# Optimization experiments

Measured on AMD Instinct MI355X. Metric: run time of the kernel, lower is better.

The kernel has to match this reference:

```python
import jax, jax.numpy as jnp
import numpy as np

N = 40000        # total points
B = 4            # batch size
Q = 256          # cfg.n_query_points
N_INSTS = B * Q  # 1024
N_MASK = 30000   # foreground points
L = 6            # cfg.dec_nlayers
LOSS_W3 = 1.0    # cfg.loss_weight[3]


def setup_inputs() -> dict:
    key = jax.random.key(0)
    k1, k2, k3, k4, k5 = jax.random.split(key, 5)
    offsets = (jnp.arange(B + 1, dtype=jnp.int32) * (N // B))
    fg_idxs = jnp.sort(jax.random.randint(k1, (N_MASK,), 0, N))
    batch_idxs = jnp.searchsorted(offsets, fg_idxs.astype(jnp.int32), side='right') - 1
    b_n = jnp.arange(N_INSTS) // Q
    fps_sampling_inds = offsets[b_n].astype(jnp.int64) + jax.random.randint(k2, (N_INSTS,), 0, N // B)
    instance_labels = jax.random.randint(k3, (N,), -1, 40)   # -1 = no instance
    semantic_labels = jax.random.randint(k4, (N,), 0, 20)    # >=4 = thing classes
    mask_logits = jax.random.normal(k5, (L, N_INSTS, N_MASK), dtype=jnp.float32)
    return {
        'mask_logits': mask_logits,
        'semantic_labels': semantic_labels,
        'instance_labels': instance_labels,
        'fg_idxs': fg_idxs,
        'batch_idxs': batch_idxs,
        'offsets': offsets,
        'fps_sampling_inds': fps_sampling_inds,
        'num_insts': N_INSTS,
    }


def reference(mask_logits, semantic_labels, instance_labels, fg_idxs,
              batch_idxs, offsets, fps_sampling_inds, num_insts):
    n_pts = instance_labels.shape[0]
    b_n = jnp.arange(num_insts) // Q                      # batch id of each query
    s_ins = instance_labels[fps_sampling_inds]            # [n_insts]
    s_seg = semantic_labels[fps_sampling_inds]            # [n_insts]
    inst_m = instance_labels[fg_idxs]                     # [n_mask]
    sem_m = semantic_labels[fg_idxs]                      # [n_mask]

    same_batch = batch_idxs[None, :] == b_n[:, None]      # [n_insts, n_mask]
    gt = inst_m[None, :] == s_ins[:, None]                # [n_insts, n_mask]

    # cover_percent: fg-point matches within query batch / all-point matches within batch slice
    num = (same_batch & gt).sum(axis=1)
    pt_batch = jnp.searchsorted(offsets, jnp.arange(n_pts, dtype=jnp.int32), side='right') - 1
    den = ((pt_batch[None, :] == b_n[:, None]) & (instance_labels[None, :] == s_ins[:, None])).sum(axis=1)
    cover = num.astype(jnp.float32) / den.astype(jnp.float32)

    positive = (s_ins >= 0) & (s_seg >= 4) & (cover >= 0.3)
    p = positive.astype(jnp.float32)                      # [n_insts]

    gt_f = gt.astype(jnp.float32)
    # weights: 1 inside own batch, zeroed where semantic label differs; rows only for positives
    w = p[:, None] * (same_batch & (sem_m[None, :] == s_seg[:, None])).astype(jnp.float32)
    w_row = w.sum(axis=1)
    counted = p * (w_row > 0).astype(jnp.float32)         # positives with >=1 valid point

    loss = jnp.float32(0.0)
    for l in range(L - 4, L):
        logit = mask_logits[l]                            # [n_insts, n_mask]
        pred = jax.nn.sigmoid(logit)
        # masked dice (weights are binary -> equals gather-then-dice of original)
        inter = (w * pred * gt_f).sum(axis=1)
        union = (w * pred * pred).sum(axis=1) + (w * gt_f).sum(axis=1) + 1e-5
        dice = 1.0 - 2.0 * inter / union
        dice_loss = (counted * dice).sum() / (counted.sum() + 1e-6)
        # weighted BCE on sigmoid (stable log-sigmoid form)
        bce = -(gt_f * jax.nn.log_sigmoid(logit) + (1.0 - gt_f) * jax.nn.log_sigmoid(-logit))
        score_loss = (bce * w).sum() / (w.sum() + 1e-6)
        loss = loss + LOSS_W3 * score_loss + dice_loss
    return loss
```

## Files before the change

### kernel.cpp

```cpp
#include <hip/hip_runtime.h>
#include <cstddef>
#include <cstdint>

#define SEMB 64
#define INSB 64
#define GRIDN 256
#define BLKN 1024
#define NWAVE 16
#define SUB 2
#define NLOSS 4
#define QPB 4
#define CHK 3840
#define MAGIC 0x5A5A5A5Au

struct Args {
    const float* logits;
    const int *sem, *inst, *fg, *bidx, *offs, *fps;
    int N, NM, NI, B, Qv, L0;
    unsigned int* flags;
    float* bceP;
    float* diceP;
    float* wcP;
    float* out;
};

__global__ __launch_bounds__(BLKN) void k_fused(Args a) {
    const int tid = threadIdx.x;
    const int bid = blockIdx.x;
    const int wid = tid >> 6, lane = tid & 63;

    __shared__ int   hA [INSB * SUB];
    __shared__ int   hFI[INSB * SUB];
    __shared__ int   hFS[SEMB * SUB];
    __shared__ int   sTot[SEMB];
    __shared__ int   lists[QPB][CHK];
    __shared__ int   lcnt[QPB];
    __shared__ int   qPos[QPB], qSi[QPB], qSs[QPB];
    __shared__ int   sFlo, sFhi;
    __shared__ float sRed[NWAVE][13];
    __shared__ float tb[NWAVE][NLOSS], td[NWAVE][NLOSS];
    __shared__ float sWC[2];

    const int b0   = (bid * QPB) / a.Qv;
    const int o_lo = a.offs[b0], o_hi = a.offs[b0 + 1];

    if (tid < INSB * SUB) { hA[tid] = 0; hFI[tid] = 0; }
    else if (tid < INSB * SUB + SEMB * SUB) hFS[tid - INSB * SUB] = 0;
    __syncthreads();

    if (tid < 896) {
        for (int k = o_lo + tid; k < o_hi; k += 896)
            atomicAdd(&hA[(a.inst[k] + 1) * SUB + (tid & (SUB - 1))], 1);
    } else if (tid == 896 || tid == 960) {
        int target = (tid == 896) ? o_lo : o_hi;
        int l_ = 0, h_ = a.NM;
        while (l_ < h_) { int m = (l_ + h_) >> 1; if (a.fg[m] < target) l_ = m + 1; else h_ = m; }
        if (tid == 896) sFlo = l_; else sFhi = l_;
    }
    __syncthreads();
    const int flo = sFlo, fhi = sFhi;

    for (int j = flo + tid; j < fhi; j += BLKN) {
        int f = a.fg[j];
        atomicAdd(&hFI[(a.inst[f] + 1) * SUB + (tid & (SUB - 1))], 1);
        atomicAdd(&hFS[a.sem[f]       * SUB + (tid & (SUB - 1))], 1);
    }
    __syncthreads();

    if (tid < SEMB) {
        int s = 0;
        for (int u = 0; u < SUB; ++u) s += hFS[tid * SUB + u];
        sTot[tid] = s;
    }
    if (tid >= 128 && tid < 128 + QPB) {
        int q = tid - 128;
        int i = bid * QPB + q;
        int pos = 0, si = -1, ss = 0;
        if (i < a.NI) {
            int fi = a.fps[i];
            si = a.inst[fi]; ss = a.sem[fi];
            if (si >= 0 && ss >= 4) {
                int num = 0, den = 0;
                for (int u = 0; u < SUB; ++u) {
                    num += hFI[(si + 1) * SUB + u];
                    den += hA [(si + 1) * SUB + u];
                }
                if ((float)num / (float)den >= 0.3f) pos = 1;
            }
        }
        qPos[q] = pos; qSi[q] = si; qSs[q] = ss;
    }
    __syncthreads();

    const int q = wid >> 2, sub = wid & 3;
    const int iq = bid * QPB + q;
    const size_t stride = (size_t)a.NI * (size_t)a.NM;
    const float* __restrict__ r0 =
        a.logits + ((size_t)a.L0 * a.NI + iq) * (size_t)a.NM;

    float acc[12];
    #pragma unroll
    for (int z = 0; z < 12; ++z) acc[z] = 0.f;
    float nm = 0.f;

    for (int c = flo; c < fhi; c += CHK) {
        int ce = (c + CHK < fhi) ? c + CHK : fhi;
        if (tid < QPB) lcnt[tid] = 0;
        __syncthreads();
        for (int j = c + tid; j < ce; j += BLKN) {
            int f  = a.fg[j];
            int sm = a.sem[f];
            int im = a.inst[f];
            int e  = j | ((im + 1) << 16);
            #pragma unroll
            for (int qq = 0; qq < QPB; ++qq) {
                if (qPos[qq] && sm == qSs[qq]) {
                    int p = atomicAdd(&lcnt[qq], 1);
                    lists[qq][p] = e;
                }
            }
        }
        __syncthreads();
        if (qPos[q]) {
            int cnt = lcnt[q];
            for (int k = (sub << 6) + lane; k < cnt; k += 256) {
                int e = lists[q][k];
                const float* __restrict__ rp = r0 + (e & 0xFFFF);
                bool g = (e >> 16) == qSi[q] + 1;
                if (g) nm += 1.f;
                #pragma unroll
                for (int l = 0; l < NLOSS; ++l) {
                    float x   = rp[(size_t)l * stride];
                    float em  = expf(-fabsf(x));
                    float inv = 1.f / (1.f + em);
                    float sg  = (x >= 0.f) ? inv : em * inv;
                    float bc  = log1pf(em) + fmaxf(x, 0.f);
                    acc[l * 3 + 0] += sg * sg;
                    if (g) { acc[l * 3 + 1] += sg; bc -= x; }
                    acc[l * 3 + 2] += bc;
                }
            }
        }
        __syncthreads();
    }

    #pragma unroll
    for (int off = 32; off > 0; off >>= 1) {
        #pragma unroll
        for (int z = 0; z < 12; ++z) acc[z] += __shfl_down(acc[z], off, 64);
        nm += __shfl_down(nm, off, 64);
    }
    if (lane == 0) {
        #pragma unroll
        for (int z = 0; z < 12; ++z) sRed[wid][z] = acc[z];
        sRed[wid][12] = nm;
    }
    __syncthreads();
    if (tid == 0) {
        float bO[NLOSS] = {0.f, 0.f, 0.f, 0.f};
        float dO[NLOSS] = {0.f, 0.f, 0.f, 0.f};
        float wr = 0.f, ct = 0.f;
        for (int qq = 0; qq < QPB; ++qq) {
            if (!qPos[qq]) continue;
            int w = sTot[qSs[qq]];
            wr += (float)w;
            ct += (w > 0) ? 1.f : 0.f;
            float s[13];
            for (int z = 0; z < 13; ++z)
                s[z] = sRed[qq * 4 + 0][z] + sRed[qq * 4 + 1][z]
                     + sRed[qq * 4 + 2][z] + sRed[qq * 4 + 3][z];
            int counted = w > 0;
            for (int l = 0; l < NLOSS; ++l) {
                bO[l] += s[l * 3 + 2];
                if (counted) {
                    float un = s[l * 3 + 0] + s[12] + 1e-5f;
                    dO[l] += 1.f - 2.f * s[l * 3 + 1] / un;
                }
            }
        }
        #pragma unroll
        for (int l = 0; l < NLOSS; ++l) {
            a.bceP[bid * NLOSS + l]  = bO[l];
            a.diceP[bid * NLOSS + l] = dO[l];
        }
        a.wcP[bid * 2 + 0] = wr;
        a.wcP[bid * 2 + 1] = ct;
        __threadfence();
        __hip_atomic_store(&a.flags[bid], MAGIC,
                           __ATOMIC_RELAXED, __HIP_MEMORY_SCOPE_AGENT);
    }

    if (bid != 0) return;

    if (wid == 0) {
        bool done = false;
        do {
            unsigned v0 = __hip_atomic_load(&a.flags[lane],       __ATOMIC_RELAXED, __HIP_MEMORY_SCOPE_AGENT);
            unsigned v1 = __hip_atomic_load(&a.flags[lane + 64],  __ATOMIC_RELAXED, __HIP_MEMORY_SCOPE_AGENT);
            unsigned v2 = __hip_atomic_load(&a.flags[lane + 128], __ATOMIC_RELAXED, __HIP_MEMORY_SCOPE_AGENT);
            unsigned v3 = __hip_atomic_load(&a.flags[lane + 192], __ATOMIC_RELAXED, __HIP_MEMORY_SCOPE_AGENT);
            done = __all((v0 == MAGIC) && (v1 == MAGIC) && (v2 == MAGIC) && (v3 == MAGIC));
            if (!done) __builtin_amdgcn_s_sleep(8);
        } while (!done);
    }
    __syncthreads();
    __threadfence();

    if (tid < GRIDN) a.flags[tid] = 0;

    float pb = a.bceP[tid], pd = a.diceP[tid];
    #pragma unroll
    for (int off = 32; off >= 4; off >>= 1) {
        pb += __shfl_down(pb, off, 64);
        pd += __shfl_down(pd, off, 64);
    }
    if (lane < NLOSS) { tb[wid][lane] = pb; td[wid][lane] = pd; }
    if (wid == 0) {
        float wv = 0.f, cv = 0.f;
        for (int b = lane; b < GRIDN; b += 64) {
            wv += a.wcP[b * 2 + 0];
            cv += a.wcP[b * 2 + 1];
        }
        #pragma unroll
        for (int off = 32; off > 0; off >>= 1) {
            wv += __shfl_down(wv, off, 64);
            cv += __shfl_down(cv, off, 64);
        }
        if (lane == 0) { sWC[0] = wv; sWC[1] = cv; }
    }
    __syncthreads();
    if (tid == 0) {
        float wsum = sWC[0] + 1e-6f;
        float csum = sWC[1] + 1e-6f;
        float loss = 0.f;
        for (int l = 0; l < NLOSS; ++l) {
            float sb = 0.f, sd = 0.f;
            for (int w = 0; w < NWAVE; ++w) { sb += tb[w][l]; sd += td[w][l]; }
            loss += sb / wsum + sd / csum;
        }
        a.out[0] = loss;
    }
}

extern "C" void kernel_launch(void* const* d_in, const int* in_sizes, int n_in,
                              void* d_out, int out_size, void* d_ws, size_t ws_size,
                              hipStream_t stream) {
    Args a;
    a.logits = (const float*)d_in[0];
    a.sem    = (const int*)d_in[1];
    a.inst   = (const int*)d_in[2];
    a.fg     = (const int*)d_in[3];
    a.bidx   = (const int*)d_in[4];
    a.offs   = (const int*)d_in[5];
    a.fps    = (const int*)d_in[6];

    a.N  = in_sizes[1];
    a.NM = in_sizes[3];
    a.NI = in_sizes[6];
    a.B  = in_sizes[5] - 1;
    const int L = (int)((long long)in_sizes[0] / ((long long)a.NI * a.NM));
    a.Qv = a.NI / a.B;
    a.L0 = L - NLOSS;

    int* ws = (int*)d_ws;
    a.flags = (unsigned int*)ws;
    a.bceP  = (float*)(ws + GRIDN);
    a.diceP = (float*)(ws + GRIDN + GRIDN * NLOSS);
    a.wcP   = (float*)(ws + GRIDN + 2 * GRIDN * NLOSS);
    a.out   = (float*)d_out;

    k_fused<<<GRIDN, BLKN, 0, stream>>>(a);
}
```

Measured before the change: 44.94 us.

## Fuse cover-ratio and weight counting into list build, dropping shared histograms

Removes the shared-memory atomic histograms over instance and semantic labels and their extra synchronised passes. The per-query denominator, numerator and weight-row counts are now accumulated in registers during the existing scan, then wave-reduced. Query positivity is decided only at the end, so candidate lists and the logit loss work are built and computed for every query, not only positive ones. The chunk size is doubled so a batch's foreground points usually fit in one chunk, at the cost of more LDS.

Result: slower. 61.42 us (+36.7%).

```diff
diff --git a/kernel.cpp b/kernel.cpp
--- a/kernel.cpp
+++ b/kernel.cpp
@@ -2,20 +2,17 @@
 #include <cstddef>
 #include <cstdint>
 
-#define SEMB 64
-#define INSB 64
 #define GRIDN 256
 #define BLKN 1024
 #define NWAVE 16
-#define SUB 2
 #define NLOSS 4
 #define QPB 4
-#define CHK 3840
+#define CHK 7680
 #define MAGIC 0x5A5A5A5Au
 
 struct Args {
     const float* logits;
-    const int *sem, *inst, *fg, *bidx, *offs, *fps;
+    const int *sem, *inst, *fg, *offs, *fps;
     int N, NM, NI, B, Qv, L0;
     unsigned int* flags;
     float* bceP;
@@ -29,71 +26,44 @@
     const int bid = blockIdx.x;
     const int wid = tid >> 6, lane = tid & 63;
 
-    __shared__ int   hA [INSB * SUB];
-    __shared__ int   hFI[INSB * SUB];
-    __shared__ int   hFS[SEMB * SUB];
-    __shared__ int   sTot[SEMB];
     __shared__ int   lists[QPB][CHK];
     __shared__ int   lcnt[QPB];
-    __shared__ int   qPos[QPB], qSi[QPB], qSs[QPB];
+    __shared__ int   qSi[QPB], qSs[QPB];
     __shared__ int   sFlo, sFhi;
     __shared__ float sRed[NWAVE][13];
+    __shared__ int   cRed[NWAVE][12];
     __shared__ float tb[NWAVE][NLOSS], td[NWAVE][NLOSS];
     __shared__ float sWC[2];
 
     const int b0   = (bid * QPB) / a.Qv;
     const int o_lo = a.offs[b0], o_hi = a.offs[b0 + 1];
 
-    if (tid < INSB * SUB) { hA[tid] = 0; hFI[tid] = 0; }
-    else if (tid < INSB * SUB + SEMB * SUB) hFS[tid - INSB * SUB] = 0;
-    __syncthreads();
-
-    if (tid < 896) {
-        for (int k = o_lo + tid; k < o_hi; k += 896)
-            atomicAdd(&hA[(a.inst[k] + 1) * SUB + (tid & (SUB - 1))], 1);
-    } else if (tid == 896 || tid == 960) {
-        int target = (tid == 896) ? o_lo : o_hi;
+    if (tid < QPB) {
+        int fi = a.fps[bid * QPB + tid];
+        qSi[tid] = a.inst[fi];
+        qSs[tid] = a.sem[fi];
+    } else if (tid == 64 || tid == 128) {
+        int target = (tid == 64) ? o_lo : o_hi;
         int l_ = 0, h_ = a.NM;
         while (l_ < h_) { int m = (l_ + h_) >> 1; if (a.fg[m] < target) l_ = m + 1; else h_ = m; }
-        if (tid == 896) sFlo = l_; else sFhi = l_;
+        if (tid == 64) sFlo = l_; else sFhi = l_;
     }
     __syncthreads();
     const int flo = sFlo, fhi = sFhi;
-
-    for (int j = flo + tid; j < fhi; j += BLKN) {
-        int f = a.fg[j];
-        atomicAdd(&hFI[(a.inst[f] + 1) * SUB + (tid & (SUB - 1))], 1);
-        atomicAdd(&hFS[a.sem[f]       * SUB + (tid & (SUB - 1))], 1);
-    }
-    __syncthreads();
-
-    if (tid < SEMB) {
-        int s = 0;
-        for (int u = 0; u < SUB; ++u) s += hFS[tid * SUB + u];
-        sTot[tid] = s;
-    }
-    if (tid >= 128 && tid < 128 + QPB) {
-        int q = tid - 128;
-        int i = bid * QPB + q;
-        int pos = 0, si = -1, ss = 0;
-        if (i < a.NI) {
-            int fi = a.fps[i];
-            si = a.inst[fi]; ss = a.sem[fi];
-            if (si >= 0 && ss >= 4) {
-                int num = 0, den = 0;
-                for (int u = 0; u < SUB; ++u) {
-                    num += hFI[(si + 1) * SUB + u];
-                    den += hA [(si + 1) * SUB + u];
-                }
-                if ((float)num / (float)den >= 0.3f) pos = 1;
-            }
-        }
-        qPos[q] = pos; qSi[q] = si; qSs[q] = ss;
-    }
-    __syncthreads();
-
+    const int si0 = qSi[0], si1 = qSi[1], si2 = qSi[2], si3 = qSi[3];
+    const int ss0 = qSs[0], ss1 = qSs[1], ss2 = qSs[2], ss3 = qSs[3];
+
+    int den0 = 0, den1 = 0, den2 = 0, den3 = 0;
+    for (int k = o_lo + tid; k < o_hi; k += BLKN) {
+        int v = a.inst[k];
+        den0 += (v == si0); den1 += (v == si1); den2 += (v == si2); den3 += (v == si3);
+    }
+
+    int num0 = 0, num1 = 0, num2 = 0, num3 = 0;
+    int wr0 = 0, wr1 = 0, wr2 = 0, wr3 = 0;
     const int q = wid >> 2, sub = wid & 3;
     const int iq = bid * QPB + q;
+    const int siq = qSi[q];
     const size_t stride = (size_t)a.NI * (size_t)a.NM;
     const float* __restrict__ r0 =
         a.logits + ((size_t)a.L0 * a.NI + iq) * (size_t)a.NM;
@@ -111,42 +81,42 @@
             int f  = a.fg[j];
             int sm = a.sem[f];
             int im = a.inst[f];
-            int e  = j | ((im + 1) << 16);
+            num0 += (im == si0); num1 += (im == si1); num2 += (im == si2); num3 += (im == si3);
+            wr0  += (sm == ss0); wr1  += (sm == ss1); wr2  += (sm == ss2); wr3  += (sm == ss3);
+            int e = j | ((im + 1) << 16);
+            if (sm == ss0) { int p = atomicAdd(&lcnt[0], 1); lists[0][p] = e; }
+            if (sm == ss1) { int p = atomicAdd(&lcnt[1], 1); lists[1][p] = e; }
+            if (sm == ss2) { int p = atomicAdd(&lcnt[2], 1); lists[2][p] = e; }
+            if (sm == ss3) { int p = atomicAdd(&lcnt[3], 1); lists[3][p] = e; }
+        }
+        __syncthreads();
+        int cnt = lcnt[q];
+        for (int k = (sub << 6) + lane; k < cnt; k += 256) {
+            int e = lists[q][k];
+            const float* __restrict__ rp = r0 + (e & 0xFFFF);
+            bool g = (e >> 16) == siq + 1;
+            if (g) nm += 1.f;
             #pragma unroll
-            for (int qq = 0; qq < QPB; ++qq) {
-                if (qPos[qq] && sm == qSs[qq]) {
-                    int p = atomicAdd(&lcnt[qq], 1);
-                    lists[qq][p] = e;
-                }
+            for (int l = 0; l < NLOSS; ++l) {
+                float x   = rp[(size_t)l * stride];
+                float em  = expf(-fabsf(x));
+                float inv = 1.f / (1.f + em);
+                float sg  = (x >= 0.f) ? inv : em * inv;
+                float bc  = log1pf(em) + fmaxf(x, 0.f);
+                acc[l * 3 + 0] += sg * sg;
+                if (g) { acc[l * 3 + 1] += sg; bc -= x; }
+                acc[l * 3 + 2] += bc;
             }
         }
         __syncthreads();
-        if (qPos[q]) {
-            int cnt = lcnt[q];
-            for (int k = (sub << 6) + lane; k < cnt; k += 256) {
-                int e = lists[q][k];
-                const float* __restrict__ rp = r0 + (e & 0xFFFF);
-                bool g = (e >> 16) == qSi[q] + 1;
-                if (g) nm += 1.f;
-                #pragma unroll
-                for (int l = 0; l < NLOSS; ++l) {
-                    float x   = rp[(size_t)l * stride];
-                    float em  = expf(-fabsf(x));
-                    float inv = 1.f / (1.f + em);
-                    float sg  = (x >= 0.f) ? inv : em * inv;
-                    float bc  = log1pf(em) + fmaxf(x, 0.f);
-                    acc[l * 3 + 0] += sg * sg;
-                    if (g) { acc[l * 3 + 1] += sg; bc -= x; }
-                    acc[l * 3 + 2] += bc;
-                }
-            }
-        }
-        __syncthreads();
-    }
-
+    }
+
+    int ci[12] = {den0, den1, den2, den3, num0, num1, num2, num3, wr0, wr1, wr2, wr3};
     #pragma unroll
     for (int off = 32; off > 0; off >>= 1) {
         #pragma unroll
+        for (int z = 0; z < 12; ++z) ci[z] += __shfl_down(ci[z], off, 64);
+        #pragma unroll
         for (int z = 0; z < 12; ++z) acc[z] += __shfl_down(acc[z], off, 64);
         nm += __shfl_down(nm, off, 64);
     }
@@ -154,25 +124,39 @@
         #pragma unroll
         for (int z = 0; z < 12; ++z) sRed[wid][z] = acc[z];
         sRed[wid][12] = nm;
+        #pragma unroll
+        for (int z = 0; z < 12; ++z) cRed[wid][z] = ci[z];
     }
     __syncthreads();
     if (tid == 0) {
+        int den[QPB] = {0,0,0,0}, num[QPB] = {0,0,0,0}, wr[QPB] = {0,0,0,0};
+        for (int w = 0; w < NWAVE; ++w)
+            for (int qq = 0; qq < QPB; ++qq) {
+                den[qq] += cRed[w][qq];
+                num[qq] += cRed[w][4 + qq];
+                wr[qq]  += cRed[w][8 + qq];
+            }
         float bO[NLOSS] = {0.f, 0.f, 0.f, 0.f};
         float dO[NLOSS] = {0.f, 0.f, 0.f, 0.f};
-        float wr = 0.f, ct = 0.f;
+        float wrS = 0.f, ctS = 0.f;
         for (int qq = 0; qq < QPB; ++qq) {
-            if (!qPos[qq]) continue;
-            int w = sTot[qSs[qq]];
-            wr += (float)w;
-            ct += (w > 0) ? 1.f : 0.f;
+            int si = qSi[qq], ss = qSs[qq];
+            int pos = 0;
+            if (si >= 0 && ss >= 4) {
+                float cover = (float)num[qq] / (float)den[qq];
+                if (cover >= 0.3f) pos = 1;
+            }
+            if (!pos) continue;
+            int w = wr[qq];
+            wrS += (float)w;
+            ctS += (w > 0) ? 1.f : 0.f;
             float s[13];
             for (int z = 0; z < 13; ++z)
                 s[z] = sRed[qq * 4 + 0][z] + sRed[qq * 4 + 1][z]
                      + sRed[qq * 4 + 2][z] + sRed[qq * 4 + 3][z];
-            int counted = w > 0;
             for (int l = 0; l < NLOSS; ++l) {
                 bO[l] += s[l * 3 + 2];
-                if (counted) {
+                if (w > 0) {
                     float un = s[l * 3 + 0] + s[12] + 1e-5f;
                     dO[l] += 1.f - 2.f * s[l * 3 + 1] / un;
                 }
@@ -183,8 +167,8 @@
             a.bceP[bid * NLOSS + l]  = bO[l];
             a.diceP[bid * NLOSS + l] = dO[l];
         }
-        a.wcP[bid * 2 + 0] = wr;
-        a.wcP[bid * 2 + 1] = ct;
+        a.wcP[bid * 2 + 0] = wrS;
+        a.wcP[bid * 2 + 1] = ctS;
         __threadfence();
         __hip_atomic_store(&a.flags[bid], MAGIC,
                            __ATOMIC_RELAXED, __HIP_MEMORY_SCOPE_AGENT);
@@ -250,7 +234,6 @@
     a.sem    = (const int*)d_in[1];
     a.inst   = (const int*)d_in[2];
     a.fg     = (const int*)d_in[3];
-    a.bidx   = (const int*)d_in[4];
     a.offs   = (const int*)d_in[5];
     a.fps    = (const int*)d_in[6];
 
```
